# Kernel tuning notes

Hardware: AMD Instinct MI355X
Metric: run time of the kernel (lower is better)

Reference implementation:

```python
import jax, jax.numpy as jnp
import numpy as np

N = 100000   # nodes
E = 800000   # directed edges
IN = 256     # in_channels (== hidden, required by repo's vn MLP dims)
HID = 256    # hidden_channels
OUT = 40     # out_channels (arxiv classes)
EPS = 1e-5


def setup_inputs() -> dict:
    key = jax.random.key(0)
    ks = jax.random.split(key, 8)
    def nrm(k, shape, scale=0.05):
        return jax.random.normal(k, shape, dtype=jnp.float32) * scale
    return {
        "x": nrm(ks[0], (N, IN), 1.0),
        "edge_index": jax.random.randint(ks[1], (2, E), 0, N, dtype=jnp.int32),
        # GCNConv weights (PyG: x @ W, then normalized aggregation, then + bias)
        "W0": nrm(ks[2], (IN, HID)),  "b0": jnp.zeros((HID,), jnp.float32),
        "W1": nrm(ks[3], (HID, HID)), "b1": jnp.zeros((HID,), jnp.float32),
        "W2": nrm(ks[4], (HID, OUT)), "b2": jnp.zeros((OUT,), jnp.float32),
        # BatchNorm1d affine params (batch-stat math, training mode)
        "bn_g0": jnp.ones((HID,), jnp.float32), "bn_b0": jnp.zeros((HID,), jnp.float32),
        "bn_g1": jnp.ones((HID,), jnp.float32), "bn_b1": jnp.zeros((HID,), jnp.float32),
        # virtual node embedding (init to 0 per reset_parameters)
        "vn_emb": jnp.zeros((1, IN), jnp.float32),
        # mlp_vns[0]: Linear(IN,HID) + LayerNorm(HID) + ReLU
        "vn_W0": nrm(ks[5], (IN, HID)),  "vn_b0": jnp.zeros((HID,), jnp.float32),
        "ln_g0": jnp.ones((HID,), jnp.float32), "ln_b0": jnp.zeros((HID,), jnp.float32),
        # mlp_vns[1]: Linear(HID,HID) + LayerNorm(HID) + ReLU
        "vn_W1": nrm(ks[6], (HID, HID)), "vn_b1": jnp.zeros((HID,), jnp.float32),
        "ln_g1": jnp.ones((HID,), jnp.float32), "ln_b1": jnp.zeros((HID,), jnp.float32),
    }


def _forward(x, edge_index, W0, b0, W1, b1, W2, b2, bn_g0, bn_b0, bn_g1, bn_b1,
             vn_emb, vn_W0, vn_b0, ln_g0, ln_b0, vn_W1, vn_b1, ln_g1, ln_b1):
    src, dst = edge_index[0], edge_index[1]
    # GCN symmetric normalization with self-loops: deg = in-degree + 1
    deg = jax.ops.segment_sum(jnp.ones(src.shape, jnp.float32), dst, num_segments=N) + 1.0
    dis = jax.lax.rsqrt(deg)                       # deg^{-1/2}  [N]
    coef = (dis[src] * dis[dst])[:, None]          # edge norm   [E,1]
    self_coef = (dis * dis)[:, None]               # self-loop norm = deg^{-1}  [N,1]

    def gcn(h, W, b):
        h = h @ W                                             # [N, out]
        agg = jax.ops.segment_sum(h[src] * coef, dst, num_segments=N)
        return agg + h * self_coef + b

    def bn(h, g, bv):  # BatchNorm1d, batch statistics over nodes
        mu = h.mean(0)
        var = ((h - mu) ** 2).mean(0)
        return (h - mu) * jax.lax.rsqrt(var + EPS) * g + bv

    def ln(h, g, bv):  # LayerNorm over last dim
        mu = h.mean(-1, keepdims=True)
        var = ((h - mu) ** 2).mean(-1, keepdims=True)
        return (h - mu) * jax.lax.rsqrt(var + EPS) * g + bv

    vx = vn_emb                                   # [1, IN]
    # layer 0
    h = x + vx                                    # virtual-node broadcast
    h = gcn(h, W0, b0)
    h = jax.nn.relu(bn(h, bn_g0, bn_b0))          # dropout = identity (eval)
    pool = jnp.sum(h, axis=0, keepdims=True)      # global_add_pool
    vx = jax.nn.relu(ln((pool + vx) @ vn_W0 + vn_b0, ln_g0, ln_b0))
    # layer 1
    h = h + vx
    h = gcn(h, W1, b1)
    h = jax.nn.relu(bn(h, bn_g1, bn_b1))
    pool = jnp.sum(h, axis=0, keepdims=True)
    vx = jax.nn.relu(ln((pool + vx) @ vn_W1 + vn_b1, ln_g1, ln_b1))
    # layer 2 (output)
    h = h + vx
    h = gcn(h, W2, b2)
    return jax.nn.log_softmax(h, axis=-1)


def reference(x, edge_index, W0, b0, W1, b1, W2, b2, bn_g0, bn_b0, bn_g1, bn_b1,
              vn_emb, vn_W0, vn_b0, ln_g0, ln_b0, vn_W1, vn_b1, ln_g1, ln_b1):
    return _forward(x, edge_index, W0, b0, W1, b1, W2, b2, bn_g0, bn_b0, bn_g1, bn_b1,
                    vn_emb, vn_W0, vn_b0, ln_g0, ln_b0, vn_W1, vn_b1, ln_g1, ln_b1)
```

## Files before the change

kernel.cpp:

```cpp
#include <hip/hip_runtime.h>
#include <hip/hip_bf16.h>
#include <cstdint>

#define N_NODES 100000
#define N_EDGES 800000
#define CH      256
#define COUT    40
#define COUTP   48
#define EPS     1e-5f
#define SCAN_CHUNK 1024
#define NSCAN_BLK  98
#define AGG_NPW 16

typedef unsigned short u16;
typedef unsigned int   u32;
typedef short s16x8 __attribute__((ext_vector_type(8)));
typedef float f32x4 __attribute__((ext_vector_type(4)));

__device__ __forceinline__ float b2f(u32 u) { return __uint_as_float(u << 16); }
__device__ __forceinline__ u16 f2b(float f) {
    u32 u = __float_as_uint(f);
    u32 r = (u + 0x7fffu + ((u >> 16) & 1u)) >> 16;
    return (u16)r;
}
__device__ __forceinline__ u32 packb(float a, float b) {
    return (u32)f2b(a) | ((u32)f2b(b) << 16);
}
__device__ __forceinline__ void unpack8(uint4 v, float* f) {
    f[0] = b2f(v.x & 0xffffu); f[1] = b2f(v.x >> 16);
    f[2] = b2f(v.y & 0xffffu); f[3] = b2f(v.y >> 16);
    f[4] = b2f(v.z & 0xffffu); f[5] = b2f(v.z >> 16);
    f[6] = b2f(v.w & 0xffffu); f[7] = b2f(v.w >> 16);
}

__global__ void k_count(const int* __restrict__ dst, int* __restrict__ counts) {
    int e = blockIdx.x * 256 + threadIdx.x;
    if (e < N_EDGES) atomicAdd(&counts[dst[e]], 1);
}

__global__ void k_scan1(const int* __restrict__ counts, int* __restrict__ partial,
                        int* __restrict__ blocksums) {
    __shared__ int sdata[256];
    int base = blockIdx.x * SCAN_CHUNK;
    int t = threadIdx.x;
    int v[4]; int s = 0;
    for (int j = 0; j < 4; j++) {
        int i = base + t * 4 + j;
        v[j] = (i < N_NODES) ? counts[i] : 0;
        s += v[j];
    }
    sdata[t] = s; __syncthreads();
    for (int off = 1; off < 256; off <<= 1) {
        int x = (t >= off) ? sdata[t - off] : 0;
        __syncthreads();
        sdata[t] += x;
        __syncthreads();
    }
    int incl = sdata[t];
    int run = incl - s;
    if (t == 255) blocksums[blockIdx.x] = incl;
    for (int j = 0; j < 4; j++) {
        int i = base + t * 4 + j;
        if (i < N_NODES) partial[i] = run;
        run += v[j];
    }
}

__global__ void k_scan2(int* __restrict__ blocksums) {
    __shared__ int sd[128];
    int t = threadIdx.x;
    int v = (t < NSCAN_BLK) ? blocksums[t] : 0;
    sd[t] = v; __syncthreads();
    for (int off = 1; off < 128; off <<= 1) {
        int x = (t >= off) ? sd[t - off] : 0;
        __syncthreads();
        sd[t] += x;
        __syncthreads();
    }
    if (t < NSCAN_BLK) blocksums[t] = sd[t] - v;
}

__global__ void k_scan3(int* __restrict__ row_start, const int* __restrict__ blocksums,
                        int* __restrict__ cursor, const int* __restrict__ counts,
                        float* __restrict__ dis) {
    int i = blockIdx.x * 256 + threadIdx.x;
    if (i < N_NODES) {
        int v = row_start[i] + blocksums[i >> 10];
        row_start[i] = v;
        cursor[i] = v;
        dis[i] = rsqrtf(1.0f + (float)counts[i]);
    }
}

__global__ void k_fill(const int* __restrict__ src, const int* __restrict__ dst,
                       int* __restrict__ cursor, int2* __restrict__ edata,
                       const float* __restrict__ dis) {
    int e = blockIdx.x * 256 + threadIdx.x;
    if (e < N_EDGES) {
        int d = dst[e], s = src[e];
        int p = atomicAdd(&cursor[d], 1);
        int2 v; v.x = s; v.y = __float_as_int(dis[s] * dis[d]);
        edata[p] = v;
    }
}

__global__ void k_wt3(const float* __restrict__ W0, const float* __restrict__ W1,
                      const float* __restrict__ W2,
                      u16* __restrict__ T0, u16* __restrict__ T1, u16* __restrict__ T2) {
    int b = blockIdx.x, k = threadIdx.x;
    if (b < 256) {
        T0[b * 256 + k] = f2b(W0[k * 256 + b]);
    } else if (b < 512) {
        int n = b - 256;
        T1[n * 256 + k] = f2b(W1[k * 256 + n]);
    } else {
        int n = b - 512;
        T2[n * 256 + k] = f2b(n < COUT ? W2[k * COUT + n] : 0.f);
    }
}

__global__ void k_vecmat(const float* __restrict__ vec, const float* __restrict__ W,
                         int ncols, int npad, float* __restrict__ outv) {
    __shared__ float s[256];
    int t = threadIdx.x;
    s[t] = vec[t];
    __syncthreads();
    float acc = 0.f;
    if (t < ncols) {
        for (int k = 0; k < 256; k++) acc += s[k] * W[k * ncols + t];
    }
    if (t < npad) outv[t] = acc;
}

__global__ __launch_bounds__(256) void k_gemm_f32a(const float* __restrict__ A,
                                                   const u16* __restrict__ Wt,
                                                   u16* __restrict__ Hout) {
    __shared__ u16 Bs[256 * 72];
    __shared__ u16 As[64 * 72];
    const int t = threadIdx.x;
    const int wave = t >> 6, lane = t & 63;
    const int lm = lane & 15, quad = lane >> 4;
    const int m0 = blockIdx.x * 64;
    const int ar = t >> 2, as_ = (t & 3) * 16;
    const int arow = m0 + ar;
    const f32x4 vz = {0.f, 0.f, 0.f, 0.f};
    f32x4 acc[4][4];
    for (int m = 0; m < 4; m++)
        for (int c = 0; c < 4; c++) acc[m][c] = vz;

    for (int k0 = 0; k0 < 256; k0 += 64) {
        {
            const uint4* bsrc = (const uint4*)(Wt + t * 256 + k0);
            uint4* bdst = (uint4*)(Bs + t * 72);
#pragma unroll
            for (int j = 0; j < 8; j++) bdst[j] = bsrc[j];
            uint4 p0 = {0,0,0,0}, p1 = {0,0,0,0};
            if (arow < N_NODES) {
                const float4* asrc = (const float4*)(A + (size_t)arow * 256 + k0 + as_);
                float4 x0 = asrc[0], x1 = asrc[1], x2 = asrc[2], x3 = asrc[3];
                p0.x = packb(x0.x, x0.y); p0.y = packb(x0.z, x0.w);
                p0.z = packb(x1.x, x1.y); p0.w = packb(x1.z, x1.w);
                p1.x = packb(x2.x, x2.y); p1.y = packb(x2.z, x2.w);
                p1.z = packb(x3.x, x3.y); p1.w = packb(x3.z, x3.w);
            }
            uint4* adst = (uint4*)(As + ar * 72 + as_);
            adst[0] = p0; adst[1] = p1;
        }
        __syncthreads();
#pragma unroll
        for (int kk = 0; kk < 64; kk += 32) {
            s16x8 af[4], bf[4];
#pragma unroll
            for (int m = 0; m < 4; m++)
                af[m] = *(const s16x8*)(As + (m * 16 + lm) * 72 + kk + quad * 8);
#pragma unroll
            for (int c = 0; c < 4; c++)
                bf[c] = *(const s16x8*)(Bs + (wave * 64 + c * 16 + lm) * 72 + kk + quad * 8);
#pragma unroll
            for (int c = 0; c < 4; c++)
#pragma unroll
                for (int m = 0; m < 4; m++)
                    acc[m][c] = __builtin_amdgcn_mfma_f32_16x16x32_bf16(af[m], bf[c], acc[m][c], 0, 0, 0);
        }
        __syncthreads();
    }
#pragma unroll
    for (int m = 0; m < 4; m++) {
#pragma unroll
        for (int c = 0; c < 4; c++) {
            int col = wave * 64 + c * 16 + lm;
#pragma unroll
            for (int i = 0; i < 4; i++) {
                int row = m0 + m * 16 + quad * 4 + i;
                if (row < N_NODES) Hout[(size_t)row * 256 + col] = f2b(acc[m][c][i]);
            }
        }
    }
}

__global__ __launch_bounds__(256) void k_gemm_bn(const u16* __restrict__ A,
                                                 const float* __restrict__ stats,
                                                 const float* __restrict__ g,
                                                 const float* __restrict__ bv,
                                                 const u16* __restrict__ Wt,
                                                 u16* __restrict__ Hout,
                                                 float* __restrict__ pool) {
    __shared__ u16 Bs[256 * 72];
    __shared__ u16 As[64 * 72];
    __shared__ float ggs[256], bcs[256], pls[256];
    const int t = threadIdx.x;
    const int wave = t >> 6, lane = t & 63;
    const int lm = lane & 15, quad = lane >> 4;
    const int m0 = blockIdx.x * 64;
    const int ar = t >> 2, as_ = (t & 3) * 16;
    const int arow = m0 + ar;
    {
        const float inv = 1.0f / (float)N_NODES;
        float mu = stats[t] * inv;
        float var = stats[256 + t] * inv - mu * mu;
        float rs = rsqrtf(var + EPS);
        float gg = g[t] * rs;
        ggs[t] = gg; bcs[t] = bv[t] - mu * gg;
        pls[t] = 0.f;
    }
    __syncthreads();
    const f32x4 vz = {0.f, 0.f, 0.f, 0.f};
    f32x4 acc[4][4];
    for (int m = 0; m < 4; m++)
        for (int c = 0; c < 4; c++) acc[m][c] = vz;

    for (int k0 = 0; k0 < 256; k0 += 64) {
        {
            const uint4* bsrc = (const uint4*)(Wt + t * 256 + k0);
            uint4* bdst = (uint4*)(Bs + t * 72);
#pragma unroll
            for (int j = 0; j < 8; j++) bdst[j] = bsrc[j];
            float f[16];
            if (arow < N_NODES) {
                const uint4* asrc = (const uint4*)(A + (size_t)arow * 256 + k0 + as_);
                uint4 r0 = asrc[0], r1 = asrc[1];
                unpack8(r0, f); unpack8(r1, f + 8);
#pragma unroll
                for (int j = 0; j < 16; j++) {
                    int c = k0 + as_ + j;
                    f[j] = fmaxf(f[j] * ggs[c] + bcs[c], 0.f);
                }
            } else {
#pragma unroll
                for (int j = 0; j < 16; j++) f[j] = 0.f;
            }
#pragma unroll
            for (int j = 0; j < 16; j++) {
                float v = f[j];
                v += __shfl_xor(v, 4);  v += __shfl_xor(v, 8);
                v += __shfl_xor(v, 16); v += __shfl_xor(v, 32);
                if (lane < 4) atomicAdd(&pls[k0 + lane * 16 + j], v);
            }
            uint4 p0, p1;
            p0.x = packb(f[0], f[1]);   p0.y = packb(f[2], f[3]);
            p0.z = packb(f[4], f[5]);   p0.w = packb(f[6], f[7]);
            p1.x = packb(f[8], f[9]);   p1.y = packb(f[10], f[11]);
            p1.z = packb(f[12], f[13]); p1.w = packb(f[14], f[15]);
            uint4* adst = (uint4*)(As + ar * 72 + as_);
            adst[0] = p0; adst[1] = p1;
        }
        __syncthreads();
#pragma unroll
        for (int kk = 0; kk < 64; kk += 32) {
            s16x8 af[4], bf[4];
#pragma unroll
            for (int m = 0; m < 4; m++)
                af[m] = *(const s16x8*)(As + (m * 16 + lm) * 72 + kk + quad * 8);
#pragma unroll
            for (int c = 0; c < 4; c++)
                bf[c] = *(const s16x8*)(Bs + (wave * 64 + c * 16 + lm) * 72 + kk + quad * 8);
#pragma unroll
            for (int c = 0; c < 4; c++)
#pragma unroll
                for (int m = 0; m < 4; m++)
                    acc[m][c] = __builtin_amdgcn_mfma_f32_16x16x32_bf16(af[m], bf[c], acc[m][c], 0, 0, 0);
        }
        __syncthreads();
    }
    atomicAdd(&pool[(blockIdx.x & 7) * 256 + t], pls[t]);
#pragma unroll
    for (int m = 0; m < 4; m++) {
#pragma unroll
        for (int c = 0; c < 4; c++) {
            int col = wave * 64 + c * 16 + lm;
#pragma unroll
            for (int i = 0; i < 4; i++) {
                int row = m0 + m * 16 + quad * 4 + i;
                if (row < N_NODES) Hout[(size_t)row * 256 + col] = f2b(acc[m][c][i]);
            }
        }
    }
}

__global__ __launch_bounds__(256) void k_gemm2_bn(const u16* __restrict__ A,
                                                  const float* __restrict__ stats,
                                                  const float* __restrict__ g,
                                                  const float* __restrict__ bv,
                                                  const u16* __restrict__ Wt,
                                                  u16* __restrict__ Hout,
                                                  float* __restrict__ pool) {
    __shared__ u16 Bs[48 * 72];
    __shared__ u16 As[64 * 72];
    __shared__ float ggs[256], bcs[256], pls[256];
    const int t = threadIdx.x;
    const int wave = t >> 6, lane = t & 63;
    const int lm = lane & 15, quad = lane >> 4;
    const int m0 = blockIdx.x * 64;
    const int ar = t >> 2, as_ = (t & 3) * 16;
    const int arow = m0 + ar;
    {
        const float inv = 1.0f / (float)N_NODES;
        float mu = stats[t] * inv;
        float var = stats[256 + t] * inv - mu * mu;
        float rs = rsqrtf(var + EPS);
        float gg = g[t] * rs;
        ggs[t] = gg; bcs[t] = bv[t] - mu * gg;
        pls[t] = 0.f;
    }
    __syncthreads();
    const f32x4 vz = {0.f, 0.f, 0.f, 0.f};
    f32x4 acc[3]; acc[0] = vz; acc[1] = vz; acc[2] = vz;

    for (int k0 = 0; k0 < 256; k0 += 64) {
        {
            if (t < 48) {
                const uint4* bsrc = (const uint4*)(Wt + t * 256 + k0);
                uint4* bdst = (uint4*)(Bs + t * 72);
#pragma unroll
                for (int j = 0; j < 8; j++) bdst[j] = bsrc[j];
            }
            float f[16];
            if (arow < N_NODES) {
                const uint4* asrc = (const uint4*)(A + (size_t)arow * 256 + k0 + as_);
                uint4 r0 = asrc[0], r1 = asrc[1];
                unpack8(r0, f); unpack8(r1, f + 8);
#pragma unroll
                for (int j = 0; j < 16; j++) {
                    int c = k0 + as_ + j;
                    f[j] = fmaxf(f[j] * ggs[c] + bcs[c], 0.f);
                }
            } else {
#pragma unroll
                for (int j = 0; j < 16; j++) f[j] = 0.f;
            }
#pragma unroll
            for (int j = 0; j < 16; j++) {
                float v = f[j];
                v += __shfl_xor(v, 4);  v += __shfl_xor(v, 8);
                v += __shfl_xor(v, 16); v += __shfl_xor(v, 32);
                if (lane < 4) atomicAdd(&pls[k0 + lane * 16 + j], v);
            }
            uint4 p0, p1;
            p0.x = packb(f[0], f[1]);   p0.y = packb(f[2], f[3]);
            p0.z = packb(f[4], f[5]);   p0.w = packb(f[6], f[7]);
            p1.x = packb(f[8], f[9]);   p1.y = packb(f[10], f[11]);
            p1.z = packb(f[12], f[13]); p1.w = packb(f[14], f[15]);
            uint4* adst = (uint4*)(As + ar * 72 + as_);
            adst[0] = p0; adst[1] = p1;
        }
        __syncthreads();
#pragma unroll
        for (int kk = 0; kk < 64; kk += 32) {
            s16x8 af = *(const s16x8*)(As + (wave * 16 + lm) * 72 + kk + quad * 8);
#pragma unroll
            for (int c = 0; c < 3; c++) {
                s16x8 bf = *(const s16x8*)(Bs + (c * 16 + lm) * 72 + kk + quad * 8);
                acc[c] = __builtin_amdgcn_mfma_f32_16x16x32_bf16(af, bf, acc[c], 0, 0, 0);
            }
        }
        __syncthreads();
    }
    atomicAdd(&pool[(blockIdx.x & 7) * 256 + t], pls[t]);
#pragma unroll
    for (int c = 0; c < 3; c++) {
        int col = c * 16 + lm;
#pragma unroll
        for (int i = 0; i < 4; i++) {
            int row = m0 + wave * 16 + quad * 4 + i;
            if (row < N_NODES) Hout[(size_t)row * COUTP + col] = f2b(acc[c][i]);
        }
    }
}

__global__ __launch_bounds__(256) void k_agg(const u16* __restrict__ H2,
                                             const int* __restrict__ row_start,
                                             const int* __restrict__ counts,
                                             const int2* __restrict__ edata,
                                             const float* __restrict__ dis,
                                             const float* __restrict__ bias,
                                             const float* __restrict__ v2,
                                             u16* __restrict__ OutB,
                                             float* __restrict__ stats) {
    __shared__ float ls[512];
    const int t = threadIdx.x, wave = t >> 6, lane = t & 63, ci = lane * 4;
    const float4 bb = *(const float4*)(bias + ci);
    const float4 vv = *(const float4*)(v2 + ci);
    float s0=0,s1=0,s2=0,s3=0,q0=0,q1=0,q2=0,q3=0;
    const int nbase = blockIdx.x * (4 * AGG_NPW) + wave * AGG_NPW;
    for (int i = 0; i < AGG_NPW; i++) {
        const int node = nbase + i;
        if (node >= N_NODES) break;
        const int beg = row_start[node], cnt = counts[node];
        const float dn = dis[node];
        float a0=0,a1=0,a2=0,a3=0, cs=0;
        int e = 0;
        for (; e + 4 <= cnt; e += 4) {
            int2 ea = edata[beg+e],   eb = edata[beg+e+1];
            int2 ec = edata[beg+e+2], ed = edata[beg+e+3];
            float ca = __int_as_float(ea.y), cb = __int_as_float(eb.y);
            float cc = __int_as_float(ec.y), cd = __int_as_float(ed.y);
            uint2 ra = *(const uint2*)(H2 + (size_t)ea.x * 256 + ci);
            uint2 rb = *(const uint2*)(H2 + (size_t)eb.x * 256 + ci);
            uint2 rc = *(const uint2*)(H2 + (size_t)ec.x * 256 + ci);
            uint2 rd = *(const uint2*)(H2 + (size_t)ed.x * 256 + ci);
            cs += ca + cb + cc + cd;
            a0 += ca*b2f(ra.x&0xffffu) + cb*b2f(rb.x&0xffffu) + cc*b2f(rc.x&0xffffu) + cd*b2f(rd.x&0xffffu);
            a1 += ca*b2f(ra.x>>16)     + cb*b2f(rb.x>>16)     + cc*b2f(rc.x>>16)     + cd*b2f(rd.x>>16);
            a2 += ca*b2f(ra.y&0xffffu) + cb*b2f(rb.y&0xffffu) + cc*b2f(rc.y&0xffffu) + cd*b2f(rd.y&0xffffu);
            a3 += ca*b2f(ra.y>>16)     + cb*b2f(rb.y>>16)     + cc*b2f(rc.y>>16)     + cd*b2f(rd.y>>16);
        }
        for (; e < cnt; e++) {
            int2 ea = edata[beg+e];
            float ca = __int_as_float(ea.y);
            uint2 ra = *(const uint2*)(H2 + (size_t)ea.x * 256 + ci);
            cs += ca;
            a0 += ca*b2f(ra.x&0xffffu); a1 += ca*b2f(ra.x>>16);
            a2 += ca*b2f(ra.y&0xffffu); a3 += ca*b2f(ra.y>>16);
        }
        uint2 rs = *(const uint2*)(H2 + (size_t)node * 256 + ci);
        const float sc = dn * dn, cv = cs + sc;
        float f0 = a0 + sc*b2f(rs.x&0xffffu) + cv*vv.x + bb.x;
        float f1 = a1 + sc*b2f(rs.x>>16)     + cv*vv.y + bb.y;
        float f2 = a2 + sc*b2f(rs.y&0xffffu) + cv*vv.z + bb.z;
        float f3 = a3 + sc*b2f(rs.y>>16)     + cv*vv.w + bb.w;
        uint2 o; o.x = packb(f0, f1); o.y = packb(f2, f3);
        *(uint2*)(OutB + (size_t)node * 256 + ci) = o;
        s0 += f0; q0 += f0*f0; s1 += f1; q1 += f1*f1;
        s2 += f2; q2 += f2*f2; s3 += f3; q3 += f3*f3;
    }
    ls[t] = 0.f; ls[256 + t] = 0.f;
    __syncthreads();
    atomicAdd(&ls[ci], s0);   atomicAdd(&ls[ci+1], s1);
    atomicAdd(&ls[ci+2], s2); atomicAdd(&ls[ci+3], s3);
    atomicAdd(&ls[256+ci], q0);   atomicAdd(&ls[256+ci+1], q1);
    atomicAdd(&ls[256+ci+2], q2); atomicAdd(&ls[256+ci+3], q3);
    __syncthreads();
    atomicAdd(&stats[t], ls[t]);
    atomicAdd(&stats[256 + t], ls[256 + t]);
}

__global__ void k_vx(const float* __restrict__ pool, const float* __restrict__ vx_old,
                     const float* __restrict__ vnW, const float* __restrict__ vnb,
                     const float* __restrict__ lng, const float* __restrict__ lnb,
                     float* __restrict__ vx_new,
                     const float* __restrict__ Wnext, int ncn, int npn,
                     float* __restrict__ v2n) {
    __shared__ float s[256];
    __shared__ float red[256];
    int t = threadIdx.x;
    float pv = 0.f;
#pragma unroll
    for (int r = 0; r < 8; r++) pv += pool[r * 256 + t];
    s[t] = pv + vx_old[t];
    __syncthreads();
    float y = vnb[t];
    for (int k = 0; k < 256; k++) y += s[k] * vnW[k * 256 + t];
    red[t] = y; __syncthreads();
    for (int off = 128; off > 0; off >>= 1) {
        if (t < off) red[t] += red[t + off];
        __syncthreads();
    }
    float mu = red[0] * (1.f / 256.f);
    __syncthreads();
    float d = y - mu;
    red[t] = d * d; __syncthreads();
    for (int off = 128; off > 0; off >>= 1) {
        if (t < off) red[t] += red[t + off];
        __syncthreads();
    }
    float var = red[0] * (1.f / 256.f);
    float v = fmaxf(d * rsqrtf(var + EPS) * lng[t] + lnb[t], 0.f);
    vx_new[t] = v;
    __syncthreads();
    s[t] = v;
    __syncthreads();
    float acc = 0.f;
    if (t < ncn) {
        for (int k = 0; k < 256; k++) acc += s[k] * Wnext[k * ncn + t];
    }
    if (t < npn) v2n[t] = acc;
}

__global__ __launch_bounds__(256) void k_agg2(const u16* __restrict__ H2,
                                              const int* __restrict__ row_start,
                                              const int* __restrict__ counts,
                                              const int2* __restrict__ edata,
                                              const float* __restrict__ dis,
                                              const float* __restrict__ bias,
                                              const float* __restrict__ v2,
                                              float* __restrict__ OutF) {
    const int t = threadIdx.x, wave = t >> 6, lane = t & 63;
    const int half = lane >> 5, hl = lane & 31;
    const bool gact = hl < 24;
    const bool cact = hl < 20;
    const int c0 = 2 * hl;
    float bb0 = 0.f, bb1 = 0.f, vv0 = 0.f, vv1 = 0.f;
    if (cact) {
        float2 bv = *(const float2*)(bias + c0); bb0 = bv.x; bb1 = bv.y;
        float2 vvv = *(const float2*)(v2 + c0);  vv0 = vvv.x; vv1 = vvv.y;
    }
    const int nbase = blockIdx.x * 16 + wave * 4;
    for (int i = 0; i < 4; i++) {
        const int node = nbase + i;
        const int beg = row_start[node], cnt = counts[node];
        const float dn = dis[node];
        float a0 = 0.f, a1 = 0.f, cs = 0.f;
        int e = half;
        for (; e + 6 < cnt; e += 8) {
            int2 ea = edata[beg+e],   eb = edata[beg+e+2];
            int2 ec = edata[beg+e+4], ed = edata[beg+e+6];
            float ca = __int_as_float(ea.y), cb = __int_as_float(eb.y);
            float cc = __int_as_float(ec.y), cd = __int_as_float(ed.y);
            u32 ra = 0, rb = 0, rc = 0, rd = 0;
            if (gact) {
                ra = *(const u32*)(H2 + (size_t)ea.x * COUTP + c0);
                rb = *(const u32*)(H2 + (size_t)eb.x * COUTP + c0);
                rc = *(const u32*)(H2 + (size_t)ec.x * COUTP + c0);
                rd = *(const u32*)(H2 + (size_t)ed.x * COUTP + c0);
            }
            cs += ca + cb + cc + cd;
            a0 += ca*b2f(ra&0xffffu) + cb*b2f(rb&0xffffu) + cc*b2f(rc&0xffffu) + cd*b2f(rd&0xffffu);
            a1 += ca*b2f(ra>>16)     + cb*b2f(rb>>16)     + cc*b2f(rc>>16)     + cd*b2f(rd>>16);
        }
        for (; e < cnt; e += 2) {
            int2 ea = edata[beg+e];
            float ca = __int_as_float(ea.y);
            u32 ra = gact ? *(const u32*)(H2 + (size_t)ea.x * COUTP + c0) : 0u;
            cs += ca;
            a0 += ca*b2f(ra&0xffffu); a1 += ca*b2f(ra>>16);
        }
        a0 += __shfl_xor(a0, 32);
        a1 += __shfl_xor(a1, 32);
        cs += __shfl_xor(cs, 32);
        const float sc = dn * dn;
        u32 rs_ = gact ? *(const u32*)(H2 + (size_t)node * COUTP + c0) : 0u;
        float h0 = a0 + sc*b2f(rs_&0xffffu) + (cs+sc)*vv0 + bb0;
        float h1 = a1 + sc*b2f(rs_>>16)     + (cs+sc)*vv1 + bb1;
        float m = cact ? fmaxf(h0, h1) : -3.0e38f;
#pragma unroll
        for (int off = 16; off > 0; off >>= 1) m = fmaxf(m, __shfl_xor(m, off));
        float ex = cact ? (expf(h0 - m) + expf(h1 - m)) : 0.f;
        float se = ex;
#pragma unroll
        for (int off = 16; off > 0; off >>= 1) se += __shfl_xor(se, off);
        float lg = logf(se);
        if (cact && half == 0) {
            float2 o = {h0 - m - lg, h1 - m - lg};
            *(float2*)(OutF + (size_t)node * COUT + c0) = o;
        }
    }
}

extern "C" void kernel_launch(void* const* d_in, const int* in_sizes, int n_in,
                              void* d_out, int out_size, void* d_ws, size_t ws_size,
                              hipStream_t stream) {
    const float* x   = (const float*)d_in[0];
    const int*   ei  = (const int*)d_in[1];
    const int*   esrc = ei;
    const int*   edst = ei + N_EDGES;
    const float* W0 = (const float*)d_in[2];  const float* b0 = (const float*)d_in[3];
    const float* W1 = (const float*)d_in[4];  const float* b1 = (const float*)d_in[5];
    const float* W2 = (const float*)d_in[6];  const float* b2 = (const float*)d_in[7];
    const float* bg0 = (const float*)d_in[8]; const float* bb0 = (const float*)d_in[9];
    const float* bg1 = (const float*)d_in[10]; const float* bb1 = (const float*)d_in[11];
    const float* vn_emb = (const float*)d_in[12];
    const float* vW0 = (const float*)d_in[13]; const float* vb0 = (const float*)d_in[14];
    const float* lg0 = (const float*)d_in[15]; const float* lb0 = (const float*)d_in[16];
    const float* vW1 = (const float*)d_in[17]; const float* vb1 = (const float*)d_in[18];
    const float* lg1 = (const float*)d_in[19]; const float* lb1 = (const float*)d_in[20];

    char* w = (char*)d_ws;
    auto alloc = [&](size_t bytes) { void* p = (void*)w; w += ((bytes + 255) / 256) * 256; return p; };
    u16* H2    = (u16*)alloc((size_t)N_NODES * 256 * 2);
    u16* OutB  = (u16*)alloc((size_t)N_NODES * 256 * 2);
    int2* edata = (int2*)alloc((size_t)N_EDGES * 8);
    int* counts = (int*)alloc((size_t)N_NODES * 4);
    int* rowst  = (int*)alloc((size_t)N_NODES * 4);
    int* cursor = (int*)alloc((size_t)N_NODES * 4);
    float* dis  = (float*)alloc((size_t)N_NODES * 4);
    u16* Wtb0 = (u16*)alloc(256 * 256 * 2);
    u16* Wtb1 = (u16*)alloc(256 * 256 * 2);
    u16* Wt2b = (u16*)alloc(COUTP * 256 * 2);
    int* scanblk = (int*)alloc(128 * 4);
    float* statsA = (float*)alloc(2560 * 4);
    float* statsB = (float*)alloc(2560 * 4);
    float* vxA = (float*)alloc(256 * 4);
    float* vxB = (float*)alloc(256 * 4);
    float* v20 = (float*)alloc(256 * 4);
    float* v21 = (float*)alloc(256 * 4);
    float* v22 = (float*)alloc(64 * 4);
    (void)ws_size; (void)in_sizes; (void)n_in; (void)out_size;

    hipMemsetAsync(counts, 0, (size_t)N_NODES * 4, stream);
    hipMemsetAsync(statsA, 0, 2560 * 4, stream);
    hipMemsetAsync(statsB, 0, 2560 * 4, stream);
    k_count<<<(N_EDGES + 255) / 256, 256, 0, stream>>>(edst, counts);
    k_scan1<<<NSCAN_BLK, 256, 0, stream>>>(counts, rowst, scanblk);
    k_scan2<<<1, 128, 0, stream>>>(scanblk);
    k_scan3<<<(N_NODES + 255) / 256, 256, 0, stream>>>(rowst, scanblk, cursor, counts, dis);
    k_fill<<<(N_EDGES + 255) / 256, 256, 0, stream>>>(esrc, edst, cursor, edata, dis);

    k_wt3<<<512 + COUTP, 256, 0, stream>>>(W0, W1, W2, Wtb0, Wtb1, Wt2b);
    k_vecmat<<<1, 256, 0, stream>>>(vn_emb, W0, 256, 256, v20);

    const int gemmblk = (N_NODES + 63) / 64;
    const int aggblk = (N_NODES + 63) / 64;

    k_gemm_f32a<<<gemmblk, 256, 0, stream>>>(x, Wtb0, H2);
    k_agg<<<aggblk, 256, 0, stream>>>(H2, rowst, counts, edata, dis, b0, v20, OutB, statsA);
    k_gemm_bn<<<gemmblk, 256, 0, stream>>>(OutB, statsA, bg0, bb0, Wtb1, H2, statsA + 512);
    k_vx<<<1, 256, 0, stream>>>(statsA + 512, vn_emb, vW0, vb0, lg0, lb0, vxA, W1, 256, 256, v21);
    k_agg<<<aggblk, 256, 0, stream>>>(H2, rowst, counts, edata, dis, b1, v21, OutB, statsB);
    k_gemm2_bn<<<gemmblk, 256, 0, stream>>>(OutB, statsB, bg1, bb1, Wt2b, H2, statsB + 512);
    k_vx<<<1, 256, 0, stream>>>(statsB + 512, vxA, vW1, vb1, lg1, lb1, vxB, W2, COUT, COUTP, v22);
    k_agg2<<<N_NODES / 16, 256, 0, stream>>>(H2, rowst, counts, edata, dis, b2, v22, (float*)d_out);
}
```

Measured before the change: 757.8 us.

## Restructure aggregation: half-wave edge split, 16-byte gathers, prefetched edge lists via shuffles

The aggregation kernel now has each half-wave process alternate edges, with every lane handling 8 channels through 16-byte loads instead of 8-byte loads. Edge indices and coefficients for a node are loaded once across the wave and broadcast with shuffles, and the next node's edge list is prefetched while the current node is being processed. Per-node metadata is loaded once per wave and shuffled to lanes. This should cut scalar edge-load latency and increase bytes in flight per gather, at the cost of cross-half reductions through shuffles, more registers, and a slower fallback path for nodes with more than 64 edges.

```diff
diff --git a/kernel.cpp b/kernel.cpp
--- a/kernel.cpp
+++ b/kernel.cpp
@@ -397,58 +397,126 @@
                                              u16* __restrict__ OutB,
                                              float* __restrict__ stats) {
     __shared__ float ls[512];
-    const int t = threadIdx.x, wave = t >> 6, lane = t & 63, ci = lane * 4;
-    const float4 bb = *(const float4*)(bias + ci);
-    const float4 vv = *(const float4*)(v2 + ci);
-    float s0=0,s1=0,s2=0,s3=0,q0=0,q1=0,q2=0,q3=0;
+    const int t = threadIdx.x, wave = t >> 6, lane = t & 63;
+    const int half = lane >> 5, hl = lane & 31;
+    const int ci = hl * 8;
+    const float4 bbA = *(const float4*)(bias + ci);
+    const float4 bbB = *(const float4*)(bias + ci + 4);
+    const float4 vvA = *(const float4*)(v2 + ci);
+    const float4 vvB = *(const float4*)(v2 + ci + 4);
+    float s[8], q[8];
+#pragma unroll
+    for (int j = 0; j < 8; j++) { s[j] = 0.f; q[j] = 0.f; }
+
     const int nbase = blockIdx.x * (4 * AGG_NPW) + wave * AGG_NPW;
+    const int nid = nbase + lane;
+    const bool nv = (lane < AGG_NPW) && (nid < N_NODES);
+    const int   my_rs = nv ? row_start[nid] : 0;
+    const int   my_ct = nv ? counts[nid] : 0;
+    const float my_dn = nv ? dis[nid] : 0.f;
+
+    int beg = __shfl(my_rs, 0), cnt = __shfl(my_ct, 0);
+    int2 my_e = {0, 0};
+    if (lane < cnt) my_e = edata[beg + lane];
+
     for (int i = 0; i < AGG_NPW; i++) {
         const int node = nbase + i;
         if (node >= N_NODES) break;
-        const int beg = row_start[node], cnt = counts[node];
-        const float dn = dis[node];
-        float a0=0,a1=0,a2=0,a3=0, cs=0;
-        int e = 0;
-        for (; e + 4 <= cnt; e += 4) {
-            int2 ea = edata[beg+e],   eb = edata[beg+e+1];
-            int2 ec = edata[beg+e+2], ed = edata[beg+e+3];
-            float ca = __int_as_float(ea.y), cb = __int_as_float(eb.y);
-            float cc = __int_as_float(ec.y), cd = __int_as_float(ed.y);
-            uint2 ra = *(const uint2*)(H2 + (size_t)ea.x * 256 + ci);
-            uint2 rb = *(const uint2*)(H2 + (size_t)eb.x * 256 + ci);
-            uint2 rc = *(const uint2*)(H2 + (size_t)ec.x * 256 + ci);
-            uint2 rd = *(const uint2*)(H2 + (size_t)ed.x * 256 + ci);
-            cs += ca + cb + cc + cd;
-            a0 += ca*b2f(ra.x&0xffffu) + cb*b2f(rb.x&0xffffu) + cc*b2f(rc.x&0xffffu) + cd*b2f(rd.x&0xffffu);
-            a1 += ca*b2f(ra.x>>16)     + cb*b2f(rb.x>>16)     + cc*b2f(rc.x>>16)     + cd*b2f(rd.x>>16);
-            a2 += ca*b2f(ra.y&0xffffu) + cb*b2f(rb.y&0xffffu) + cc*b2f(rc.y&0xffffu) + cd*b2f(rd.y&0xffffu);
-            a3 += ca*b2f(ra.y>>16)     + cb*b2f(rb.y>>16)     + cc*b2f(rc.y>>16)     + cd*b2f(rd.y>>16);
-        }
-        for (; e < cnt; e++) {
-            int2 ea = edata[beg+e];
-            float ca = __int_as_float(ea.y);
-            uint2 ra = *(const uint2*)(H2 + (size_t)ea.x * 256 + ci);
-            cs += ca;
-            a0 += ca*b2f(ra.x&0xffffu); a1 += ca*b2f(ra.x>>16);
-            a2 += ca*b2f(ra.y&0xffffu); a3 += ca*b2f(ra.y>>16);
-        }
-        uint2 rs = *(const uint2*)(H2 + (size_t)node * 256 + ci);
+        const int2 cur_e = my_e;
+        const int  ccnt = cnt, cbeg = beg;
+        const float dn = __shfl(my_dn, i);
+        const uint4 rs_ = *(const uint4*)(H2 + (size_t)node * 256 + ci);
+        if (i + 1 < AGG_NPW && node + 1 < N_NODES) {
+            beg = __shfl(my_rs, i + 1);
+            cnt = __shfl(my_ct, i + 1);
+            int2 tmp = {0, 0};
+            if (lane < cnt) tmp = edata[beg + lane];
+            my_e = tmp;
+        }
+        const int cnt64 = ccnt < 64 ? ccnt : 64;
+        const int cnt8 = (cnt64 + 7) & ~7;
+        float a[8];
+#pragma unroll
+        for (int j = 0; j < 8; j++) a[j] = 0.f;
+        float cs = 0.f;
+        for (int e = 0; e < cnt8; e += 8) {
+            const int   si0 = __shfl(cur_e.x, e + half);
+            const int   si1 = __shfl(cur_e.x, e + 2 + half);
+            const int   si2 = __shfl(cur_e.x, e + 4 + half);
+            const int   si3 = __shfl(cur_e.x, e + 6 + half);
+            const float cf0 = __int_as_float(__shfl(cur_e.y, e + half));
+            const float cf1 = __int_as_float(__shfl(cur_e.y, e + 2 + half));
+            const float cf2 = __int_as_float(__shfl(cur_e.y, e + 4 + half));
+            const float cf3 = __int_as_float(__shfl(cur_e.y, e + 6 + half));
+            const uint4 r0 = *(const uint4*)(H2 + (size_t)si0 * 256 + ci);
+            const uint4 r1 = *(const uint4*)(H2 + (size_t)si1 * 256 + ci);
+            const uint4 r2 = *(const uint4*)(H2 + (size_t)si2 * 256 + ci);
+            const uint4 r3 = *(const uint4*)(H2 + (size_t)si3 * 256 + ci);
+            cs += cf0 + cf1 + cf2 + cf3;
+            a[0] += cf0*b2f(r0.x&0xffffu) + cf1*b2f(r1.x&0xffffu) + cf2*b2f(r2.x&0xffffu) + cf3*b2f(r3.x&0xffffu);
+            a[1] += cf0*b2f(r0.x>>16)     + cf1*b2f(r1.x>>16)     + cf2*b2f(r2.x>>16)     + cf3*b2f(r3.x>>16);
+            a[2] += cf0*b2f(r0.y&0xffffu) + cf1*b2f(r1.y&0xffffu) + cf2*b2f(r2.y&0xffffu) + cf3*b2f(r3.y&0xffffu);
+            a[3] += cf0*b2f(r0.y>>16)     + cf1*b2f(r1.y>>16)     + cf2*b2f(r2.y>>16)     + cf3*b2f(r3.y>>16);
+            a[4] += cf0*b2f(r0.z&0xffffu) + cf1*b2f(r1.z&0xffffu) + cf2*b2f(r2.z&0xffffu) + cf3*b2f(r3.z&0xffffu);
+            a[5] += cf0*b2f(r0.z>>16)     + cf1*b2f(r1.z>>16)     + cf2*b2f(r2.z>>16)     + cf3*b2f(r3.z>>16);
+            a[6] += cf0*b2f(r0.w&0xffffu) + cf1*b2f(r1.w&0xffffu) + cf2*b2f(r2.w&0xffffu) + cf3*b2f(r3.w&0xffffu);
+            a[7] += cf0*b2f(r0.w>>16)     + cf1*b2f(r1.w>>16)     + cf2*b2f(r2.w>>16)     + cf3*b2f(r3.w>>16);
+        }
+        if (ccnt > 64) {
+            int e2 = 64;
+            for (; e2 + 2 <= ccnt; e2 += 2) {
+                const int2 ed_ = edata[cbeg + e2 + half];
+                const float cf = __int_as_float(ed_.y);
+                const uint4 r = *(const uint4*)(H2 + (size_t)ed_.x * 256 + ci);
+                cs += cf;
+                a[0] += cf*b2f(r.x&0xffffu); a[1] += cf*b2f(r.x>>16);
+                a[2] += cf*b2f(r.y&0xffffu); a[3] += cf*b2f(r.y>>16);
+                a[4] += cf*b2f(r.z&0xffffu); a[5] += cf*b2f(r.z>>16);
+                a[6] += cf*b2f(r.w&0xffffu); a[7] += cf*b2f(r.w>>16);
+            }
+            if (e2 < ccnt && half == 0) {
+                const int2 ed_ = edata[cbeg + e2];
+                const float cf = __int_as_float(ed_.y);
+                const uint4 r = *(const uint4*)(H2 + (size_t)ed_.x * 256 + ci);
+                cs += cf;
+                a[0] += cf*b2f(r.x&0xffffu); a[1] += cf*b2f(r.x>>16);
+                a[2] += cf*b2f(r.y&0xffffu); a[3] += cf*b2f(r.y>>16);
+                a[4] += cf*b2f(r.z&0xffffu); a[5] += cf*b2f(r.z>>16);
+                a[6] += cf*b2f(r.w&0xffffu); a[7] += cf*b2f(r.w>>16);
+            }
+        }
+        cs += __shfl_xor(cs, 32);
+#pragma unroll
+        for (int j = 0; j < 8; j++) a[j] += __shfl_xor(a[j], 32);
         const float sc = dn * dn, cv = cs + sc;
-        float f0 = a0 + sc*b2f(rs.x&0xffffu) + cv*vv.x + bb.x;
-        float f1 = a1 + sc*b2f(rs.x>>16)     + cv*vv.y + bb.y;
-        float f2 = a2 + sc*b2f(rs.y&0xffffu) + cv*vv.z + bb.z;
-        float f3 = a3 + sc*b2f(rs.y>>16)     + cv*vv.w + bb.w;
-        uint2 o; o.x = packb(f0, f1); o.y = packb(f2, f3);
-        *(uint2*)(OutB + (size_t)node * 256 + ci) = o;
-        s0 += f0; q0 += f0*f0; s1 += f1; q1 += f1*f1;
-        s2 += f2; q2 += f2*f2; s3 += f3; q3 += f3*f3;
+        const float f0 = a[0] + sc*b2f(rs_.x&0xffffu) + cv*vvA.x + bbA.x;
+        const float f1 = a[1] + sc*b2f(rs_.x>>16)     + cv*vvA.y + bbA.y;
+        const float f2 = a[2] + sc*b2f(rs_.y&0xffffu) + cv*vvA.z + bbA.z;
+        const float f3 = a[3] + sc*b2f(rs_.y>>16)     + cv*vvA.w + bbA.w;
+        const float f4 = a[4] + sc*b2f(rs_.z&0xffffu) + cv*vvB.x + bbB.x;
+        const float f5 = a[5] + sc*b2f(rs_.z>>16)     + cv*vvB.y + bbB.y;
+        const float f6 = a[6] + sc*b2f(rs_.w&0xffffu) + cv*vvB.z + bbB.z;
+        const float f7 = a[7] + sc*b2f(rs_.w>>16)     + cv*vvB.w + bbB.w;
+        if (half == 0) {
+            uint4 o;
+            o.x = packb(f0, f1); o.y = packb(f2, f3);
+            o.z = packb(f4, f5); o.w = packb(f6, f7);
+            *(uint4*)(OutB + (size_t)node * 256 + ci) = o;
+        }
+        s[0] += f0; q[0] += f0*f0;  s[1] += f1; q[1] += f1*f1;
+        s[2] += f2; q[2] += f2*f2;  s[3] += f3; q[3] += f3*f3;
+        s[4] += f4; q[4] += f4*f4;  s[5] += f5; q[5] += f5*f5;
+        s[6] += f6; q[6] += f6*f6;  s[7] += f7; q[7] += f7*f7;
     }
     ls[t] = 0.f; ls[256 + t] = 0.f;
     __syncthreads();
-    atomicAdd(&ls[ci], s0);   atomicAdd(&ls[ci+1], s1);
-    atomicAdd(&ls[ci+2], s2); atomicAdd(&ls[ci+3], s3);
-    atomicAdd(&ls[256+ci], q0);   atomicAdd(&ls[256+ci+1], q1);
-    atomicAdd(&ls[256+ci+2], q2); atomicAdd(&ls[256+ci+3], q3);
+    if (half == 0) {
+#pragma unroll
+        for (int j = 0; j < 8; j++) {
+            atomicAdd(&ls[ci + j], s[j]);
+            atomicAdd(&ls[256 + ci + j], q[j]);
+        }
+    }
     __syncthreads();
     atomicAdd(&stats[t], ls[t]);
     atomicAdd(&stats[256 + t], ls[256 + t]);
```

New measurement: 735.6 us. 1.03x faster.
